# Kernel optimization log

Measured on AMD Instinct MI355X. Metric: run time of the kernel, lower is better.

The kernel has to match this reference:

```python
import jax, jax.numpy as jnp
import numpy as np

C = 128

def setup_inputs() -> dict:
    key = jax.random.key(0)
    ks = jax.random.split(key, 7)
    x = jax.random.normal(ks[0], (4, 64, 64, C), dtype=jnp.float32)
    s = 1.0 / np.sqrt(C)
    Wq = jax.random.normal(ks[1], (C, C), dtype=jnp.float32) * s
    bq = jnp.zeros((C,), dtype=jnp.float32)
    Wk = jax.random.normal(ks[2], (C, C), dtype=jnp.float32) * s
    bk = jnp.zeros((C,), dtype=jnp.float32)
    Wv = jax.random.normal(ks[3], (C, C), dtype=jnp.float32) * s
    bv = jnp.zeros((C,), dtype=jnp.float32)
    return {"x": x, "Wq": Wq, "bq": bq, "Wk": Wk, "bk": bk, "Wv": Wv, "bv": bv}

def reference(x, Wq, bq, Wk, bk, Wv, bv):
    B, H, W, Cc = x.shape
    N = H * W
    xt = x.reshape(B, N, Cc)  # 1x1 conv == per-token linear
    q = xt @ Wq + bq
    k = xt @ Wk + bk
    v = xt @ Wv + bv
    scale = jnp.sqrt(jnp.asarray(Cc, dtype=x.dtype))
    attn = jnp.einsum('bnc,bmc->bnm', q, k) / scale  # [B, N, N]
    attn = jax.nn.softmax(attn, axis=-1)
    out = jnp.einsum('bnm,bmc->bnc', attn, v)
    return x + out.reshape(B, H, W, Cc)
```

## Files before the change

### kernel.cpp

```cpp
#include <hip/hip_runtime.h>

constexpr int C       = 128;
constexpr int N       = 4096;
constexpr int BATCH   = 4;
constexpr int TOTROWS = BATCH * N;
constexpr float SCALE = 0.08838834764831845f;
constexpr float LOG2E = 1.44269504088896340736f;

constexpr int BK = 64;

typedef __attribute__((ext_vector_type(8))) short        bf16x8;
typedef __attribute__((ext_vector_type(4))) float        f32x4;
typedef __attribute__((ext_vector_type(2))) unsigned int u32x2;

__device__ inline unsigned short f2bf(float f) {
    unsigned int u = __float_as_uint(f);
    return (unsigned short)((u + 0x7FFFu + ((u >> 16) & 1u)) >> 16);
}
__device__ inline unsigned int cvtpk(float a, float b) {
    unsigned int r;
    asm("v_cvt_pk_bf16_f32 %0, %1, %2" : "=v"(r) : "v"(a), "v"(b));
    return r;
}
__device__ inline float bf2f(unsigned int u) {
    return __uint_as_float(u << 16);
}
__device__ inline float fexp2(float x) {
#if __has_builtin(__builtin_amdgcn_exp2f)
    return __builtin_amdgcn_exp2f(x);
#else
    float r; asm("v_exp_f32 %0, %1\n\ts_nop 0" : "=v"(r) : "v"(x)); return r;
#endif
}
__device__ inline void dma16(const void* g, void* l) {
    __builtin_amdgcn_global_load_lds(
        (const __attribute__((address_space(1))) void*)g,
        (__attribute__((address_space(3))) void*)l, 16, 0, 0);
}

__global__ __launch_bounds__(256)
void wprep_kernel(const float* __restrict__ Wq, const float* __restrict__ Wk,
                  const float* __restrict__ Wv, unsigned short* __restrict__ wt)
{
    const int mat = blockIdx.x;
    const float* W = (mat == 0) ? Wq : (mat == 1) ? Wk : Wv;
    const float  s = (mat == 0) ? SCALE * LOG2E : 1.0f;
    unsigned short* dst = wt + mat * 16384;

    const int t  = threadIdx.x;
    const int o  = t >> 1;
    const int g0 = (t & 1) * 8;
    const int xr = (o >> 2) & 7;
    #pragma unroll
    for (int gg = 0; gg < 8; ++gg) {
        const int g   = g0 + gg;
        const int ihi = (g & 8) | ((g & 7) ^ xr);
        const int i0  = ihi << 3;
        union { unsigned short u16[8]; uint4 v; } buf;
        #pragma unroll
        for (int e = 0; e < 8; ++e)
            buf.u16[e] = f2bf(W[(i0 + e) * 128 + o] * s);
        *reinterpret_cast<uint4*>(&dst[o * 128 + g * 8]) = buf.v;
    }
}

__global__ __launch_bounds__(256, 2)
void qkv_kernel(const float* __restrict__ x, const unsigned short* __restrict__ wt,
                const float* __restrict__ bq, const float* __restrict__ bk,
                const float* __restrict__ bv,
                unsigned short* __restrict__ qo,
                unsigned short* __restrict__ ko,
                unsigned short* __restrict__ vt)
{
    __shared__ __align__(16) unsigned short wl[16384];

    const int tid  = threadIdx.x;
    const int lane = tid & 63;
    const int lo   = lane & 15;
    const int quad = lane >> 4;
    const int mat  = blockIdx.y;
    const long rowbase = (long)blockIdx.x * 64 + (tid >> 6) * 16;

    {
        const char* src = (const char*)(wt + mat * 16384);
        #pragma unroll
        for (int c = 0; c < 8; ++c)
            dma16(src + (c * 256 + tid) * 16, &wl[(c * 256 + tid) * 8]);
    }

    bf16x8 xf[4];
    {
        const float4* xr = reinterpret_cast<const float4*>(&x[(rowbase + lo) * C]);
        #pragma unroll
        for (int ks = 0; ks < 4; ++ks) {
            float4 a  = xr[ks * 8 + quad * 2];
            float4 b2 = xr[ks * 8 + quad * 2 + 1];
            union { bf16x8 v; unsigned int u[4]; } cv;
            cv.u[0] = cvtpk(a.x, a.y);
            cv.u[1] = cvtpk(a.z, a.w);
            cv.u[2] = cvtpk(b2.x, b2.y);
            cv.u[3] = cvtpk(b2.z, b2.w);
            xf[ks] = cv.v;
        }
    }

    __syncthreads();

    if (mat < 2) {
        f32x4 acc[8] = {};
        #pragma unroll
        for (int ks = 0; ks < 4; ++ks)
            #pragma unroll
            for (int mt = 0; mt < 8; ++mt) {
                const int rr = mt * 16 + lo;
                bf16x8 wf = *reinterpret_cast<const bf16x8*>(
                    &wl[rr * 128 + (((ks * 4 + quad) ^ ((rr >> 2) & 7)) << 3)]);
                acc[mt] = __builtin_amdgcn_mfma_f32_16x16x32_bf16(
                    wf, xf[ks], acc[mt], 0, 0, 0);
            }
        const float* bias = (mat == 0) ? bq : bk;
        const float  s    = (mat == 0) ? SCALE * LOG2E : 1.0f;
        unsigned short* out = (mat == 0) ? qo : ko;
        long row = rowbase + lo;
        #pragma unroll
        for (int mt = 0; mt < 8; ++mt) {
            float4 bb = *reinterpret_cast<const float4*>(&bias[mt * 16 + quad * 4]);
            u32x2 w;
            w[0] = cvtpk(acc[mt][0] + bb.x * s, acc[mt][1] + bb.y * s);
            w[1] = cvtpk(acc[mt][2] + bb.z * s, acc[mt][3] + bb.w * s);
            *reinterpret_cast<u32x2*>(&out[row * C + mt * 16 + quad * 4]) = w;
        }
    } else {
        f32x4 acc[8] = {};
        #pragma unroll
        for (int ks = 0; ks < 4; ++ks)
            #pragma unroll
            for (int ct = 0; ct < 8; ++ct) {
                const int rr = ct * 16 + lo;
                bf16x8 wf = *reinterpret_cast<const bf16x8*>(
                    &wl[rr * 128 + (((ks * 4 + quad) ^ ((rr >> 2) & 7)) << 3)]);
                acc[ct] = __builtin_amdgcn_mfma_f32_16x16x32_bf16(
                    xf[ks], wf, acc[ct], 0, 0, 0);
            }
        const int b = (int)(rowbase >> 12);
        const int nbase = (int)(rowbase & (N - 1));
        const int n0   = nbase + quad * 4;
        const int nblk = n0 >> 6;
        #pragma unroll
        for (int ct = 0; ct < 8; ++ct) {
            int chan = ct * 16 + lo;
            float bb = bv[chan];
            u32x2 w;
            w[0] = cvtpk(acc[ct][0] + bb, acc[ct][1] + bb);
            w[1] = cvtpk(acc[ct][2] + bb, acc[ct][3] + bb);
            *reinterpret_cast<u32x2*>(
                &vt[(((size_t)b * 64 + nblk) * 128 + chan) * 64 + (n0 & 63)]) = w;
        }
    }
}

__global__ __launch_bounds__(256, 2)
void attn_kernel(const unsigned short* __restrict__ q,
                 const unsigned short* __restrict__ k,
                 const unsigned short* __restrict__ vt,
                 unsigned short* __restrict__ opart,
                 float* __restrict__ lpart)
{
    __shared__ __align__(16) unsigned short smA[17472];
    __shared__ __align__(16) unsigned short smB[16384];
    __shared__ __align__(16) unsigned short smP[4096];

    const int tid  = threadIdx.x;
    const int wv   = tid >> 6;
    const int lane = tid & 63;
    const int lo   = lane & 15;
    const int quad = lane >> 4;

    const int nspl = (int)(gridDim.x >> 7);
    const int id   = blockIdx.x;
    int b, sl, qt;
    if (nspl == 4) {
        b  = (id >> 1) & 3;
        sl = (id & 1) | (((id >> 3) & 1) << 1);
        qt = id >> 4;
    } else {
        b  = (id >> 1) & 3;
        sl = id & 1;
        qt = id >> 3;
    }
    const int NIT  = (N / nspl) / BK;
    const int koff = sl * (N / nspl);

    const int    rowb  = b * N + qt * 128;
    const size_t qrow0 = (size_t)rowb + wv * 32;
    const char* kb8 = (const char*)(k  + ((size_t)b * N + koff) * C);
    const char* vb8 = (const char*)(vt + ((size_t)b * 64 + (koff >> 6)) * (size_t)(128 * 64));

    unsigned short* PW = smP + wv * 1024;

    bf16x8 qf[2][4];
    #pragma unroll
    for (int nt = 0; nt < 2; ++nt)
        #pragma unroll
        for (int ks = 0; ks < 4; ++ks)
            qf[nt][ks] = *reinterpret_cast<const bf16x8*>(
                &q[(qrow0 + nt * 16 + lo) * C + ks * 32 + quad * 8]);

    int offK[4], offV[4];
    #pragma unroll
    for (int c = 0; c < 4; ++c) {
        int G  = (wv * 4 + c) * 64 + lane;
        int kr = G >> 4;
        offK[c] = kr * 256 + (((G & 15) ^ (kr & 7)) << 4);
        int vr = G >> 3;
        offV[c] = vr * 128 + (((G & 7) ^ (vr & 7)) << 4);
    }

    auto stage = [&](int kt, unsigned short* dstKV) {
        const char* kt8 = kb8 + kt * 16384;
        const char* vt8 = vb8 + kt * 16384;
        #pragma unroll
        for (int c = 0; c < 4; ++c)
            dma16(kt8 + offK[c], dstKV + (wv * 4 + c) * 512);
        #pragma unroll
        for (int c = 0; c < 4; ++c)
            dma16(vt8 + offV[c], dstKV + 8192 + (wv * 4 + c) * 512);
    };

    float l_i[2] = { 0.f, 0.f };
    f32x4 ot[2][8] = {};

    auto body = [&](const unsigned short* base) {
        const unsigned short* kc = base;
        const unsigned short* vc = base + 8192;

        f32x4 st[4][2] = {};
        #pragma unroll
        for (int ks = 0; ks < 4; ++ks)
            #pragma unroll
            for (int mt = 0; mt < 4; ++mt) {
                const bf16x8 kf = *reinterpret_cast<const bf16x8*>(
                    &kc[(mt * 16 + lo) * 128 + (((ks * 4 + quad) ^ (lo & 7)) << 3)]);
                #pragma unroll
                for (int nt = 0; nt < 2; ++nt)
                    st[mt][nt] = __builtin_amdgcn_mfma_f32_16x16x32_bf16(
                        kf, qf[nt][ks], st[mt][nt], 0, 0, 0);
            }

        #pragma unroll
        for (int h = 0; h < 2; ++h) {
            #pragma unroll
            for (int nt = 0; nt < 2; ++nt) {
                const int prow = nt * 16 + lo;
                float ps = 0.f;
                #pragma unroll
                for (int m = 0; m < 2; ++m) {
                    f32x4 s = st[2 * h + m][nt];
                    float p0 = fexp2(s[0]);
                    float p1 = fexp2(s[1]);
                    float p2 = fexp2(s[2]);
                    float p3 = fexp2(s[3]);
                    ps += (p0 + p1) + (p2 + p3);
                    u32x2 w;
                    w[0] = cvtpk(p0, p1);
                    w[1] = cvtpk(p2, p3);
                    *reinterpret_cast<u32x2*>(
                        &PW[prow * 32 + (((2 * m + (quad >> 1)) ^ (prow & 3)) << 3)
                            + (quad & 1) * 4]) = w;
                }
                l_i[nt] += ps;
            }
            bf16x8 pf[2];
            #pragma unroll
            for (int nt = 0; nt < 2; ++nt) {
                const int prow = nt * 16 + lo;
                pf[nt] = *reinterpret_cast<const bf16x8*>(
                    &PW[prow * 32 + ((quad ^ (prow & 3)) << 3)]);
            }
            #pragma unroll
            for (int ct = 0; ct < 8; ++ct) {
                const bf16x8 vf = *reinterpret_cast<const bf16x8*>(
                    &vc[(ct * 16 + lo) * 64 + (((h * 4 + quad) ^ (lo & 7)) << 3)]);
                #pragma unroll
                for (int nt = 0; nt < 2; ++nt)
                    ot[nt][ct] = __builtin_amdgcn_mfma_f32_16x16x32_bf16(
                        vf, pf[nt], ot[nt][ct], 0, 0, 0);
            }
        }
    };

    stage(0, smA);
    __syncthreads();
    for (int kt = 0; kt < NIT; kt += 2) {
        stage(kt + 1, smB);
        body(smA);
        __syncthreads();
        if (kt + 2 < NIT) stage(kt + 2, smA);
        body(smB);
        __syncthreads();
    }

    #pragma unroll
    for (int nt = 0; nt < 2; ++nt) {
        l_i[nt] += __shfl_xor(l_i[nt], 16);
        l_i[nt] += __shfl_xor(l_i[nt], 32);
    }
    if (quad == 0) {
        #pragma unroll
        for (int nt = 0; nt < 2; ++nt)
            lpart[(size_t)sl * TOTROWS + qrow0 + nt * 16 + lo] = l_i[nt];
    }

    constexpr int OSTR = 136;
    unsigned short* obl = smA;
    #pragma unroll
    for (int nt = 0; nt < 2; ++nt) {
        const int row = wv * 32 + nt * 16 + lo;
        #pragma unroll
        for (int ct = 0; ct < 8; ++ct) {
            u32x2 w;
            w[0] = cvtpk(ot[nt][ct][0], ot[nt][ct][1]);
            w[1] = cvtpk(ot[nt][ct][2], ot[nt][ct][3]);
            *reinterpret_cast<u32x2*>(&obl[row * OSTR + ct * 16 + quad * 4]) = w;
        }
    }
    __syncthreads();
    {
        unsigned short* obg = opart + (size_t)sl * TOTROWS * C;
        const int row  = tid >> 1;
        const int half = tid & 1;
        const unsigned short* src = &obl[row * OSTR + half * 64];
        unsigned short*       dst = &obg[((size_t)rowb + row) * C + half * 64];
        #pragma unroll
        for (int i = 0; i < 8; ++i)
            *reinterpret_cast<uint4*>(&dst[i * 8]) =
                *reinterpret_cast<const uint4*>(&src[i * 8]);
    }
}

__global__ __launch_bounds__(256)
void combine_kernel(const float* __restrict__ x,
                    const unsigned short* __restrict__ opart,
                    const float* __restrict__ lpart,
                    float* __restrict__ out, int nspl)
{
    int gid = blockIdx.x * 256 + threadIdx.x;
    int row = gid >> 4;
    int c8  = (gid & 15) * 8;

    float denom = 0.f;
    for (int j = 0; j < nspl; ++j) denom += lpart[(size_t)j * TOTROWS + row];
    float inv = 1.0f / denom;

    size_t idx = (size_t)row * C + c8;
    float a[8] = {};
    for (int j = 0; j < nspl; ++j) {
        uint4 o = *reinterpret_cast<const uint4*>(
            &opart[(size_t)j * TOTROWS * C + idx]);
        a[0] += bf2f(o.x & 0xffff);  a[1] += bf2f(o.x >> 16);
        a[2] += bf2f(o.y & 0xffff);  a[3] += bf2f(o.y >> 16);
        a[4] += bf2f(o.z & 0xffff);  a[5] += bf2f(o.z >> 16);
        a[6] += bf2f(o.w & 0xffff);  a[7] += bf2f(o.w >> 16);
    }
    float4 xv0 = *reinterpret_cast<const float4*>(&x[idx]);
    float4 xv1 = *reinterpret_cast<const float4*>(&x[idx + 4]);
    float4 o0, o1;
    o0.x = xv0.x + a[0] * inv;  o0.y = xv0.y + a[1] * inv;
    o0.z = xv0.z + a[2] * inv;  o0.w = xv0.w + a[3] * inv;
    o1.x = xv1.x + a[4] * inv;  o1.y = xv1.y + a[5] * inv;
    o1.z = xv1.z + a[6] * inv;  o1.w = xv1.w + a[7] * inv;
    *reinterpret_cast<float4*>(&out[idx])     = o0;
    *reinterpret_cast<float4*>(&out[idx + 4]) = o1;
}

extern "C" void kernel_launch(void* const* d_in, const int* in_sizes, int n_in,
                              void* d_out, int out_size, void* d_ws, size_t ws_size,
                              hipStream_t stream)
{
    const float* x  = (const float*)d_in[0];
    const float* Wq = (const float*)d_in[1];
    const float* bq = (const float*)d_in[2];
    const float* Wk = (const float*)d_in[3];
    const float* bk = (const float*)d_in[4];
    const float* Wv = (const float*)d_in[5];
    const float* bv = (const float*)d_in[6];
    float* out = (float*)d_out;

    const int nspl = (ws_size >= ((size_t)31 << 20)) ? 4 : 2;

    const size_t SPLIT_BYTES = (size_t)TOTROWS * C * 2;
    char* ws = (char*)d_ws;
    unsigned short* opart = (unsigned short*)ws;
    char* base = ws + (size_t)nspl * SPLIT_BYTES;
    unsigned short* q  = (unsigned short*)(base);
    unsigned short* k  = (unsigned short*)(base + SPLIT_BYTES);
    unsigned short* vt = (unsigned short*)(base + 2 * SPLIT_BYTES);
    float*          lp = (float*)(base + 3 * SPLIT_BYTES);
    unsigned short* wt = (unsigned short*)(base + 3 * SPLIT_BYTES
                                           + (size_t)nspl * TOTROWS * 4);

    wprep_kernel<<<3, 256, 0, stream>>>(Wq, Wk, Wv, wt);
    qkv_kernel<<<dim3(TOTROWS / 64, 3), 256, 0, stream>>>(
        x, wt, bq, bk, bv, q, k, vt);
    attn_kernel<<<nspl * 128, 256, 0, stream>>>(q, k, vt, opart, lp);
    combine_kernel<<<TOTROWS * 16 / 256, 256, 0, stream>>>(x, opart, lp, out, nspl);
}
```

Before: 128.6 us.

## Split attention work across 8 waves with shared P tile in LDS

The attention kernel moves from 256 to 512 threads per block. Each pair of waves shares 32 query rows: one half computes scores for half of each key tile and also handles half of the output channels for P·V. The probabilities go into a block-shared LDS tile, which adds a __syncthreads inside every body iteration. Partial row sums are reduced through LDS before being written. The aim is lower register pressure per wave and more waves per CU to hide latency, at the cost of extra barriers.

```diff
diff --git a/kernel.cpp b/kernel.cpp
--- a/kernel.cpp
+++ b/kernel.cpp
@@ -159,22 +159,22 @@
     }
 }
 
-__global__ __launch_bounds__(256, 2)
+__global__ __launch_bounds__(512, 4)
 void attn_kernel(const unsigned short* __restrict__ q,
                  const unsigned short* __restrict__ k,
                  const unsigned short* __restrict__ vt,
                  unsigned short* __restrict__ opart,
                  float* __restrict__ lpart)
 {
-    __shared__ __align__(16) unsigned short smA[17472];
-    __shared__ __align__(16) unsigned short smB[16384];
-    __shared__ __align__(16) unsigned short smP[4096];
+    __shared__ __align__(16) unsigned short sm[40960];
 
     const int tid  = threadIdx.x;
     const int wv   = tid >> 6;
     const int lane = tid & 63;
     const int lo   = lane & 15;
     const int quad = lane >> 4;
+    const int wr   = wv & 3;
+    const int wh   = wv >> 2;
 
     const int nspl = (int)(gridDim.x >> 7);
     const int id   = blockIdx.x;
@@ -192,11 +192,14 @@
     const int koff = sl * (N / nspl);
 
     const int    rowb  = b * N + qt * 128;
-    const size_t qrow0 = (size_t)rowb + wv * 32;
+    const size_t qrow0 = (size_t)rowb + wr * 32;
+    const int    rloc0 = wr * 32;
+    const int    khbase = wh * 32;
+    const int    chbase = wh * 64;
     const char* kb8 = (const char*)(k  + ((size_t)b * N + koff) * C);
     const char* vb8 = (const char*)(vt + ((size_t)b * 64 + (koff >> 6)) * (size_t)(128 * 64));
 
-    unsigned short* PW = smP + wv * 1024;
+    unsigned short* pl = sm + 32768;
 
     bf16x8 qf[2][4];
     #pragma unroll
@@ -206,10 +209,10 @@
             qf[nt][ks] = *reinterpret_cast<const bf16x8*>(
                 &q[(qrow0 + nt * 16 + lo) * C + ks * 32 + quad * 8]);
 
-    int offK[4], offV[4];
+    int offK[2], offV[2];
     #pragma unroll
-    for (int c = 0; c < 4; ++c) {
-        int G  = (wv * 4 + c) * 64 + lane;
+    for (int c = 0; c < 2; ++c) {
+        int G  = c * 512 + tid;
         int kr = G >> 4;
         offK[c] = kr * 256 + (((G & 15) ^ (kr & 7)) << 4);
         int vr = G >> 3;
@@ -220,67 +223,72 @@
         const char* kt8 = kb8 + kt * 16384;
         const char* vt8 = vb8 + kt * 16384;
         #pragma unroll
-        for (int c = 0; c < 4; ++c)
-            dma16(kt8 + offK[c], dstKV + (wv * 4 + c) * 512);
-        #pragma unroll
-        for (int c = 0; c < 4; ++c)
-            dma16(vt8 + offV[c], dstKV + 8192 + (wv * 4 + c) * 512);
+        for (int c = 0; c < 2; ++c)
+            dma16(kt8 + offK[c], dstKV + (c * 512 + tid) * 8);
+        #pragma unroll
+        for (int c = 0; c < 2; ++c)
+            dma16(vt8 + offV[c], dstKV + 8192 + (c * 512 + tid) * 8);
     };
 
     float l_i[2] = { 0.f, 0.f };
-    f32x4 ot[2][8] = {};
+    f32x4 ot[2][4] = {};
 
     auto body = [&](const unsigned short* base) {
         const unsigned short* kc = base;
         const unsigned short* vc = base + 8192;
 
-        f32x4 st[4][2] = {};
+        f32x4 st[2][2] = {};
         #pragma unroll
         for (int ks = 0; ks < 4; ++ks)
             #pragma unroll
-            for (int mt = 0; mt < 4; ++mt) {
+            for (int m = 0; m < 2; ++m) {
                 const bf16x8 kf = *reinterpret_cast<const bf16x8*>(
-                    &kc[(mt * 16 + lo) * 128 + (((ks * 4 + quad) ^ (lo & 7)) << 3)]);
+                    &kc[(khbase + m * 16 + lo) * 128
+                        + (((ks * 4 + quad) ^ (lo & 7)) << 3)]);
                 #pragma unroll
                 for (int nt = 0; nt < 2; ++nt)
-                    st[mt][nt] = __builtin_amdgcn_mfma_f32_16x16x32_bf16(
-                        kf, qf[nt][ks], st[mt][nt], 0, 0, 0);
-            }
-
-        #pragma unroll
-        for (int h = 0; h < 2; ++h) {
+                    st[m][nt] = __builtin_amdgcn_mfma_f32_16x16x32_bf16(
+                        kf, qf[nt][ks], st[m][nt], 0, 0, 0);
+            }
+
+        #pragma unroll
+        for (int nt = 0; nt < 2; ++nt) {
+            const int prow = rloc0 + nt * 16 + lo;
+            float ps = 0.f;
+            #pragma unroll
+            for (int m = 0; m < 2; ++m) {
+                f32x4 s = st[m][nt];
+                float p0 = fexp2(s[0]);
+                float p1 = fexp2(s[1]);
+                float p2 = fexp2(s[2]);
+                float p3 = fexp2(s[3]);
+                ps += (p0 + p1) + (p2 + p3);
+                u32x2 w;
+                w[0] = cvtpk(p0, p1);
+                w[1] = cvtpk(p2, p3);
+                const int g = wh * 4 + m * 2 + (quad >> 1);
+                *reinterpret_cast<u32x2*>(
+                    &pl[prow * 64 + ((g ^ (prow & 7)) << 3) + (quad & 1) * 4]) = w;
+            }
+            l_i[nt] += ps;
+        }
+
+        __syncthreads();
+
+        #pragma unroll
+        for (int ks2 = 0; ks2 < 2; ++ks2) {
+            bf16x8 pf[2];
             #pragma unroll
             for (int nt = 0; nt < 2; ++nt) {
-                const int prow = nt * 16 + lo;
-                float ps = 0.f;
-                #pragma unroll
-                for (int m = 0; m < 2; ++m) {
-                    f32x4 s = st[2 * h + m][nt];
-                    float p0 = fexp2(s[0]);
-                    float p1 = fexp2(s[1]);
-                    float p2 = fexp2(s[2]);
-                    float p3 = fexp2(s[3]);
-                    ps += (p0 + p1) + (p2 + p3);
-                    u32x2 w;
-                    w[0] = cvtpk(p0, p1);
-                    w[1] = cvtpk(p2, p3);
-                    *reinterpret_cast<u32x2*>(
-                        &PW[prow * 32 + (((2 * m + (quad >> 1)) ^ (prow & 3)) << 3)
-                            + (quad & 1) * 4]) = w;
-                }
-                l_i[nt] += ps;
-            }
-            bf16x8 pf[2];
-            #pragma unroll
-            for (int nt = 0; nt < 2; ++nt) {
-                const int prow = nt * 16 + lo;
+                const int prow = rloc0 + nt * 16 + lo;
                 pf[nt] = *reinterpret_cast<const bf16x8*>(
-                    &PW[prow * 32 + ((quad ^ (prow & 3)) << 3)]);
-            }
-            #pragma unroll
-            for (int ct = 0; ct < 8; ++ct) {
+                    &pl[prow * 64 + (((ks2 * 4 + quad) ^ (prow & 7)) << 3)]);
+            }
+            #pragma unroll
+            for (int ct = 0; ct < 4; ++ct) {
                 const bf16x8 vf = *reinterpret_cast<const bf16x8*>(
-                    &vc[(ct * 16 + lo) * 64 + (((h * 4 + quad) ^ (lo & 7)) << 3)]);
+                    &vc[(chbase + ct * 16 + lo) * 64
+                        + (((ks2 * 4 + quad) ^ (lo & 7)) << 3)]);
                 #pragma unroll
                 for (int nt = 0; nt < 2; ++nt)
                     ot[nt][ct] = __builtin_amdgcn_mfma_f32_16x16x32_bf16(
@@ -289,14 +297,14 @@
         }
     };
 
-    stage(0, smA);
+    stage(0, sm);
     __syncthreads();
     for (int kt = 0; kt < NIT; kt += 2) {
-        stage(kt + 1, smB);
-        body(smA);
+        stage(kt + 1, sm + 16384);
+        body(sm);
         __syncthreads();
-        if (kt + 2 < NIT) stage(kt + 2, smA);
-        body(smB);
+        if (kt + 2 < NIT) stage(kt + 2, sm);
+        body(sm + 16384);
         __syncthreads();
     }
 
@@ -305,36 +313,44 @@
         l_i[nt] += __shfl_xor(l_i[nt], 16);
         l_i[nt] += __shfl_xor(l_i[nt], 32);
     }
+    float* lred = (float*)(sm + 20480);
     if (quad == 0) {
         #pragma unroll
         for (int nt = 0; nt < 2; ++nt)
-            lpart[(size_t)sl * TOTROWS + qrow0 + nt * 16 + lo] = l_i[nt];
+            lred[wh * 128 + rloc0 + nt * 16 + lo] = l_i[nt];
     }
 
     constexpr int OSTR = 136;
-    unsigned short* obl = smA;
+    unsigned short* obl = sm;
     #pragma unroll
     for (int nt = 0; nt < 2; ++nt) {
-        const int row = wv * 32 + nt * 16 + lo;
-        #pragma unroll
-        for (int ct = 0; ct < 8; ++ct) {
+        const int row = rloc0 + nt * 16 + lo;
+        #pragma unroll
+        for (int ct = 0; ct < 4; ++ct) {
             u32x2 w;
             w[0] = cvtpk(ot[nt][ct][0], ot[nt][ct][1]);
             w[1] = cvtpk(ot[nt][ct][2], ot[nt][ct][3]);
-            *reinterpret_cast<u32x2*>(&obl[row * OSTR + ct * 16 + quad * 4]) = w;
+            *reinterpret_cast<u32x2*>(
+                &obl[row * OSTR + chbase + ct * 16 + quad * 4]) = w;
         }
     }
     __syncthreads();
     {
         unsigned short* obg = opart + (size_t)sl * TOTROWS * C;
-        const int row  = tid >> 1;
-        const int half = tid & 1;
-        const unsigned short* src = &obl[row * OSTR + half * 64];
-        unsigned short*       dst = &obg[((size_t)rowb + row) * C + half * 64];
-        #pragma unroll
-        for (int i = 0; i < 8; ++i)
+        const int row = tid >> 2;
+        const int qtr = tid & 3;
+        const unsigned short* src = &obl[row * OSTR + qtr * 32];
+        unsigned short*       dst = &obg[((size_t)rowb + row) * C + qtr * 32];
+        #pragma unroll
+        for (int i = 0; i < 4; ++i)
             *reinterpret_cast<uint4*>(&dst[i * 8]) =
                 *reinterpret_cast<const uint4*>(&src[i * 8]);
+    }
+    if (wh == 0 && quad == 0) {
+        #pragma unroll
+        for (int nt = 0; nt < 2; ++nt)
+            lpart[(size_t)sl * TOTROWS + qrow0 + nt * 16 + lo] =
+                l_i[nt] + lred[128 + rloc0 + nt * 16 + lo];
     }
 }
 
@@ -402,6 +418,6 @@
     wprep_kernel<<<3, 256, 0, stream>>>(Wq, Wk, Wv, wt);
     qkv_kernel<<<dim3(TOTROWS / 64, 3), 256, 0, stream>>>(
         x, wt, bq, bk, bv, q, k, vt);
-    attn_kernel<<<nspl * 128, 256, 0, stream>>>(q, k, vt, opart, lp);
+    attn_kernel<<<nspl * 128, 512, 0, stream>>>(q, k, vt, opart, lp);
     combine_kernel<<<TOTROWS * 16 / 256, 256, 0, stream>>>(x, opart, lp, out, nspl);
 }
```

New measurement: 134.6 us. 4.6% more time.
